# Kernel optimization log

Hardware: AMD Instinct MI355X
Metric: run time of the kernel (lower is better)

## Reference

```python
import jax, jax.numpy as jnp
import numpy as np

N_AGENTS = 8; N_DUMMY = 16; BATCH = 1024; PLAN = 128; HID = 256

def setup_inputs():
    key = jax.random.key(0)
    ks = jax.random.split(key, 12)
    N, ND, B, P, H = N_AGENTS, N_DUMMY, BATCH, PLAN, HID
    plans = jax.random.normal(ks[0], (B, N, P), jnp.float32)
    keep = jax.random.bernoulli(ks[1], 0.7, (B, N))  # ragged communication pattern
    comm_plans = jax.random.normal(ks[2], (B, N, P), jnp.float32) * keep[:, :, None]
    coord_hiddens = 0.1 * jax.random.normal(ks[3], (N, 2, B, H), jnp.float32)
    dummy_noise = jax.random.normal(ks[4], (N, ND - N, B, 2 * P), jnp.float32)
    s = 0.05
    Wi_f = s * jax.random.normal(ks[5], (N, 3 * H, 2 * P), jnp.float32)
    Wh_f = s * jax.random.normal(ks[6], (N, 3 * H, H), jnp.float32)
    Wi_b = s * jax.random.normal(ks[7], (N, 3 * H, 2 * P), jnp.float32)
    Wh_b = s * jax.random.normal(ks[8], (N, 3 * H, H), jnp.float32)
    ln_g = jnp.ones((N, 2 * H), jnp.float32)
    ln_b = jnp.zeros((N, 2 * H), jnp.float32)
    W1 = s * jax.random.normal(ks[9], (N, H, 2 * H), jnp.float32)
    b1 = jnp.zeros((N, H), jnp.float32)
    W2 = s * jax.random.normal(ks[10], (N, 2, H), jnp.float32)
    b2 = jnp.zeros((N, 2), jnp.float32)
    return dict(plans=plans, comm_plans=comm_plans, coord_hiddens=coord_hiddens,
                dummy_noise=dummy_noise, Wi_f=Wi_f, Wh_f=Wh_f, Wi_b=Wi_b, Wh_b=Wh_b,
                ln_g=ln_g, ln_b=ln_b, W1=W1, b1=b1, W2=W2, b2=b2)

def _gru_scan(xs, h0, Wi, Wh, valid):
    # PyTorch GRU cell (biases are zero-initialized in RecurrentHead), length-masked
    H = h0.shape[-1]
    gi_all = jnp.einsum('tbi,gi->tbg', xs, Wi)  # (T,B,3H) input projections, one GEMM
    def step(h, inp):
        gi, v = inp
        gh = h @ Wh.T
        r = jax.nn.sigmoid(gi[:, :H] + gh[:, :H])
        z = jax.nn.sigmoid(gi[:, H:2 * H] + gh[:, H:2 * H])
        n = jnp.tanh(gi[:, 2 * H:] + r * gh[:, 2 * H:])
        hn = (1.0 - z) * n + z * h
        h = jnp.where(v[:, None], hn, h)            # packed: no update past seq end
        return h, jnp.where(v[:, None], hn, 0.0)    # pad_packed returns zeros there
    hT, out = jax.lax.scan(step, h0, (gi_all, valid))
    return out, hT

def _forward(plans, comm_plans, coord_hiddens, dummy_noise, Wi_f, Wh_f, Wi_b, Wh_b, ln_g, ln_b, W1, b1, W2, b2):
    B, N, P = plans.shape
    ND = N_DUMMY
    # comm_plans[~any(any(comm_plans))] = plans[...]
    empty = ~jnp.any(jnp.any(comm_plans != 0, -1), -1)            # (B,)
    comm = jnp.where(empty[:, None, None], plans, comm_plans)     # (B,N,P)
    mask_real = jnp.any(comm != 0, -1).T                          # (N,B)
    mask = jnp.concatenate([mask_real, jnp.ones((ND - N, B), bool)], 0)  # (ND,B)
    mask_flat = mask.reshape(-1)
    seq_len = mask.sum(0)                                         # (B,)
    t_idx = jnp.arange(ND)[:, None]
    packed_mask = t_idx < seq_len[None, :]                        # (ND,B)
    pm_flat = packed_mask.reshape(-1)
    # torch boolean-index / masked_scatter consume elements in flat row-major order;
    # we reproduce those exact semantics.
    src_idx = jnp.nonzero(mask_flat, size=ND * B, fill_value=0)[0]
    rank_pack = jnp.cumsum(pm_flat) - 1
    cum_scat = jnp.cumsum(mask_flat) - 1
    rev_idx = jnp.where(packed_mask, seq_len[None, :] - 1 - t_idx, 0)

    def pack(x):  # compact_seq[packed_mask] = x[batch_mask]
        xf = x.reshape(ND * B, -1)
        return jnp.where(pm_flat[:, None], xf[src_idx[rank_pack]], 0.0).reshape(ND, B, -1)

    def scatter(s):  # zeros.masked_scatter(mask, scores)
        st, sb = cum_scat // B, cum_scat % B
        return jnp.where(mask_flat[:, None], s[st, sb], 0.0).reshape(ND, B, -1)

    def rev(a):  # per-column reversal within valid length (for bidirectional GRU)
        g = jnp.take_along_axis(a, jnp.broadcast_to(rev_idx[:, :, None], a.shape), axis=0)
        return jnp.where(packed_mask[:, :, None], g, 0.0)

    plans_t = plans.transpose(1, 0, 2)  # (N,B,P): plans[:, i] per agent

    def per_agent(plan_i, dn_i, hxs_i, wif, whf, wib, whb, g, bta, w1, bb1, w2, bb2):
        others = jnp.concatenate([jnp.broadcast_to(plan_i[:, None, :], comm.shape), comm], -1)  # (B,N,2P)
        x = jnp.concatenate([others.transpose(1, 0, 2), dn_i], 0)  # (ND,B,2P) with randn dummy rows
        cseq = pack(x)
        out_f, hf = _gru_scan(cseq, hxs_i[0], wif, whf, packed_mask)
        out_b_r, hb = _gru_scan(rev(cseq), hxs_i[1], wib, whb, packed_mask)
        out_b = rev(out_b_r)
        scores = scatter(jnp.concatenate([out_f, out_b], -1))  # (ND,B,2H)
        mu = scores.mean(-1, keepdims=True)
        var = ((scores - mu) ** 2).mean(-1, keepdims=True)
        scores = (scores - mu) * jax.lax.rsqrt(var + 1e-5) * g + bta  # LayerNorm
        h1 = jax.nn.relu(jnp.einsum('tbc,hc->tbh', scores, w1) + bb1)
        cm = jnp.einsum('tbh,oh->tbo', h1, w2) + bb2               # (ND,B,2)
        return cm, jnp.stack([hf, hb])                              # (2,B,H)

    coord_masks, coord_rnn_hxs = jax.vmap(per_agent)(
        plans_t, dummy_noise, coord_hiddens, Wi_f, Wh_f, Wi_b, Wh_b, ln_g, ln_b, W1, b1, W2, b2)
    return coord_masks, coord_rnn_hxs

def reference(plans, comm_plans, coord_hiddens, dummy_noise, Wi_f, Wh_f, Wi_b, Wh_b, ln_g, ln_b, W1, b1, W2, b2):
    return _forward(plans, comm_plans, coord_hiddens, dummy_noise, Wi_f, Wh_f, Wi_b, Wh_b, ln_g, ln_b, W1, b1, W2, b2)
```

## Files before the change

### kernel.cpp

```cpp
#include <hip/hip_runtime.h>


typedef _Float16 f16;
typedef __attribute__((ext_vector_type(4))) _Float16 f16x4;
typedef __attribute__((ext_vector_type(8))) _Float16 f16x8;
typedef __attribute__((ext_vector_type(4))) float floatx4;

__device__ __forceinline__ float sigf(float x) { return 1.0f / (1.0f + __expf(-x)); }
__device__ __forceinline__ float tanhfast(float x) {
    float e = __expf(2.0f * x);
    return 1.0f - 2.0f / (e + 1.0f);
}

__device__ __forceinline__ void gl16(const f16* g, f16* l) {
    __builtin_amdgcn_global_load_lds((const __attribute__((address_space(1))) void*)g,
                                     (__attribute__((address_space(3))) void*)l,
                                     16, 0, 0);
}

__global__ void k_empty(const float* __restrict__ comm, int* __restrict__ empty) {
    int b = blockIdx.x;
    __shared__ int flag;
    if (threadIdx.x == 0) flag = 0;
    __syncthreads();
    const float* p = comm + (size_t)b * 1024;
    int any = 0;
    for (int e = threadIdx.x; e < 1024; e += 256)
        if (p[e] != 0.0f) any = 1;
    if (any) flag = 1;
    __syncthreads();
    if (threadIdx.x == 0) empty[b] = (flag == 0);
}

__global__ void k_mask(const float* __restrict__ plans, const float* __restrict__ comm,
                       const int* __restrict__ empty, int* __restrict__ mask) {
    int row = blockIdx.x * 4 + (threadIdx.x >> 6);
    int lane = threadIdx.x & 63;
    int t = row >> 10, b = row & 1023;
    int m;
    if (t >= 8) {
        m = 1;
    } else {
        const float* src = (empty[b] ? plans : comm) + ((size_t)b * 8 + t) * 128;
        float v0 = src[lane * 2], v1 = src[lane * 2 + 1];
        m = __any((v0 != 0.0f) || (v1 != 0.0f)) ? 1 : 0;
    }
    if (lane == 0) mask[row] = m;
}

__global__ void k_scan(const int* __restrict__ mask, int* __restrict__ seq_len,
                       int* __restrict__ pack_src, int* __restrict__ scat_src,
                       int* __restrict__ inv_scat) {
    __shared__ int s_sl[1024];
    __shared__ int s_m[1024];
    __shared__ int s_p[1024];
    __shared__ unsigned short s_idx[16384];
    int tid = threadIdx.x;
    int sl = 8;
    for (int t = 0; t < 8; t++) sl += mask[t * 1024 + tid];
    s_sl[tid] = sl;
    seq_len[tid] = sl;
    __syncthreads();
    int mv[16], pv[16];
    int mc = 0, pc = 0;
    int j0 = tid * 16;
    for (int q = 0; q < 16; q++) {
        int j = j0 + q;
        mv[q] = mask[j];
        pv[q] = ((j >> 10) < s_sl[j & 1023]) ? 1 : 0;
        mc += mv[q]; pc += pv[q];
    }
    s_m[tid] = mc; s_p[tid] = pc;
    __syncthreads();
    for (int off = 1; off < 1024; off <<= 1) {
        int am = (tid >= off) ? s_m[tid - off] : 0;
        int ap = (tid >= off) ? s_p[tid - off] : 0;
        __syncthreads();
        s_m[tid] += am; s_p[tid] += ap;
        __syncthreads();
    }
    if (tid == 1023) seq_len[1024] = s_m[1023];
    int moff = s_m[tid] - mc;
    int poff = s_p[tid] - pc;
    int rm = moff;
    for (int q = 0; q < 16; q++)
        if (mv[q]) s_idx[rm++] = (unsigned short)(j0 + q);
    __syncthreads();
    rm = moff;
    int rp = poff;
    for (int q = 0; q < 16; q++) {
        int j = j0 + q;
        scat_src[j] = mv[q] ? rm : -1;
        if (mv[q]) { inv_scat[rm] = j; rm++; }
        pack_src[j] = pv[q] ? (int)s_idx[rp] : -1;
        if (pv[q]) rp++;
    }
}

__global__ void k_pack(const float* __restrict__ plans, const float* __restrict__ comm,
                       const float* __restrict__ dummy, const int* __restrict__ empty,
                       const int* __restrict__ pack_src, f16* __restrict__ cseq) {
    int row = blockIdx.x * 8 + (threadIdx.x >> 5);
    int lane = threadIdx.x & 31;
    int i = row >> 14;
    int j = row & 16383;
    int s = pack_src[j];
    f16x8 o = {0, 0, 0, 0, 0, 0, 0, 0};
    if (s >= 0) {
        int tp = s >> 10, bp = s & 1023;
        const float* src;
        if (tp < 8) {
            if (lane < 16) src = plans + ((size_t)bp * 8 + i) * 128 + lane * 8;
            else src = (empty[bp] ? plans : comm) + ((size_t)bp * 8 + tp) * 128 + (lane - 16) * 8;
        } else {
            src = dummy + (((size_t)i * 8 + (tp - 8)) * 1024 + bp) * 256 + lane * 8;
        }
        float4 v0 = *(const float4*)src;
        float4 v1 = *(const float4*)(src + 4);
        o[0] = (f16)v0.x; o[1] = (f16)v0.y; o[2] = (f16)v0.z; o[3] = (f16)v0.w;
        o[4] = (f16)v1.x; o[5] = (f16)v1.y; o[6] = (f16)v1.z; o[7] = (f16)v1.w;
    }
    *(f16x8*)(cseq + ((size_t)row << 8) + lane * 8) = o;
}

__global__ void k_prep_w(const float* __restrict__ Wi_f, const float* __restrict__ Wh_f,
                         const float* __restrict__ Wi_b, const float* __restrict__ Wh_b,
                         f16* __restrict__ whalf) {
    int ch2 = blockIdx.y;
    int ch = ch2 >> 1, sel = ch2 & 1;
    int i = ch >> 1, d = ch & 1;
    const float* src = sel ? (d ? Wh_b : Wh_f) : (d ? Wi_b : Wi_f);
    src += (size_t)i * 196608;
    int off = (blockIdx.x * 256 + threadIdx.x) * 4;
    float4 v = *(const float4*)(src + off);
    f16x4 o = { (f16)v.x, (f16)v.y, (f16)v.z, (f16)v.w };
    *(f16x4*)(whalf + (size_t)ch2 * 196608 + off) = o;
}

__global__ void k_prep_w1(const float* __restrict__ W1, f16* __restrict__ w1half) {
    int off = (blockIdx.x * 256 + threadIdx.x) * 4;
    float4 v = *(const float4*)(W1 + off);
    f16x4 o = { (f16)v.x, (f16)v.y, (f16)v.z, (f16)v.w };
    *(f16x4*)(w1half + off) = o;
}

__global__ void k_init_h(const float* __restrict__ hx, float* __restrict__ h,
                         f16* __restrict__ hh0) {
    int e = (blockIdx.x * 256 + threadIdx.x) * 4;
    float4 v = *(const float4*)(hx + e);
    *(float4*)(h + e) = v;
    f16x4 o = { (f16)v.x, (f16)v.y, (f16)v.z, (f16)v.w };
    *(f16x4*)(hh0 + e) = o;
}

__global__ void k_zfill(const int* __restrict__ scat_src, const int* __restrict__ seq_len,
                        f16* __restrict__ scores) {
    int j = blockIdx.x;
    int tid = threadIdx.x;
    int c = scat_src[j];
    if (c < 0) {
        for (int i = 0; i < 8; i++) {
            unsigned int* p = (unsigned int*)(scores + ((size_t)(i * 16384 + j)) * 512);
            p[tid] = 0u;
        }
    } else {
        int st = c >> 10, sb = c & 1023;
        if (st >= seq_len[sb] && tid < 128) {
            for (int i = 0; i < 8; i++) {
                unsigned int* p = (unsigned int*)(scores + ((size_t)(i * 16384 + j)) * 512 + 256);
                p[tid] = 0u;
            }
        }
    }
}

__global__ __launch_bounds__(256, 2) void k_step(
    const f16* __restrict__ cseq, const f16* __restrict__ whalf,
    float* __restrict__ h, const f16* __restrict__ hh_in, f16* __restrict__ hh_out,
    f16* __restrict__ scores, const int* __restrict__ seq_len,
    const int* __restrict__ inv_scat, int t)
{
    __shared__ f16 lA[128 * 64];
    __shared__ f16 lB[192 * 64];
    int bx = blockIdx.x;
    int ch = bx >> 5;
    int mt = (bx >> 2) & 7;
    int nt = bx & 3;
    int i = ch >> 1, d = ch & 1;
    int tid = threadIdx.x;
    int lane = tid & 63, w = tid >> 6;
    int li = lane & 15, q = lane >> 4;
    int rsub = lane >> 3;
    int sc = (lane & 7) ^ rsub;

    const f16* pA[4]; const f16* pH[4]; const f16* pB[6];
#pragma unroll
    for (int p = 0; p < 4; p++) {
        int ar = (w * 4 + p) * 8 + rsub;
        int b = mt * 128 + ar;
        int tt = t;
        if (d) { int sl = seq_len[b]; tt = sl - 1 - t; if (tt < 0) tt = 0; }
        pA[p] = cseq + (((size_t)i * 16 + tt) * 1024 + b) * 256 + sc * 8;
        pH[p] = hh_in + ((size_t)ch * 1024 + b) * 256 + sc * 8;
    }
#pragma unroll
    for (int p = 0; p < 6; p++) {
        int nr = (w * 6 + p) * 8 + rsub;
        int g = (nr >> 6) * 256 + nt * 64 + (nr & 63);
        pB[p] = whalf + (size_t)(ch * 2) * 196608 + (size_t)g * 256 + sc * 8;
    }

    floatx4 accr[4][2], accz[4][2], accgi[4][2], accgh[4][2];
    floatx4 z4 = {0.f, 0.f, 0.f, 0.f};
#pragma unroll
    for (int n = 0; n < 4; n++)
        for (int s = 0; s < 2; s++) { accr[n][s] = z4; accz[n][s] = z4; accgi[n][s] = z4; accgh[n][s] = z4; }

    for (int kt = 0; kt < 512; kt += 64) {
        bool xph = (kt < 256);
        if (xph) {
#pragma unroll
            for (int p = 0; p < 4; p++) gl16(pA[p] + kt, &lA[(w * 4 + p) * 512]);
#pragma unroll
            for (int p = 0; p < 6; p++) gl16(pB[p] + kt, &lB[(w * 6 + p) * 512]);
        } else {
#pragma unroll
            for (int p = 0; p < 4; p++) gl16(pH[p] + (kt - 256), &lA[(w * 4 + p) * 512]);
#pragma unroll
            for (int p = 0; p < 6; p++) gl16(pB[p] + 196608 + (kt - 256), &lB[(w * 6 + p) * 512]);
        }
        __syncthreads();
#pragma unroll
        for (int kk = 0; kk < 64; kk += 32) {
            int sw = ((q + (kk >> 3)) ^ (li & 7)) << 3;
            f16x8 a0 = *(f16x8*)&lA[(w * 32 + li) * 64 + sw];
            f16x8 a1 = *(f16x8*)&lA[(w * 32 + 16 + li) * 64 + sw];
#pragma unroll
            for (int n = 0; n < 4; n++) {
                f16x8 br = *(f16x8*)&lB[(n * 16 + li) * 64 + sw];
                f16x8 bz = *(f16x8*)&lB[(64 + n * 16 + li) * 64 + sw];
                f16x8 bn = *(f16x8*)&lB[(128 + n * 16 + li) * 64 + sw];
                accr[n][0] = __builtin_amdgcn_mfma_f32_16x16x32_f16(a0, br, accr[n][0], 0, 0, 0);
                accr[n][1] = __builtin_amdgcn_mfma_f32_16x16x32_f16(a1, br, accr[n][1], 0, 0, 0);
                accz[n][0] = __builtin_amdgcn_mfma_f32_16x16x32_f16(a0, bz, accz[n][0], 0, 0, 0);
                accz[n][1] = __builtin_amdgcn_mfma_f32_16x16x32_f16(a1, bz, accz[n][1], 0, 0, 0);
                if (xph) {
                    accgi[n][0] = __builtin_amdgcn_mfma_f32_16x16x32_f16(a0, bn, accgi[n][0], 0, 0, 0);
                    accgi[n][1] = __builtin_amdgcn_mfma_f32_16x16x32_f16(a1, bn, accgi[n][1], 0, 0, 0);
                } else {
                    accgh[n][0] = __builtin_amdgcn_mfma_f32_16x16x32_f16(a0, bn, accgh[n][0], 0, 0, 0);
                    accgh[n][1] = __builtin_amdgcn_mfma_f32_16x16x32_f16(a1, bn, accgh[n][1], 0, 0, 0);
                }
            }
        }
        __syncthreads();
    }

    int T = seq_len[1024];
#pragma unroll
    for (int s = 0; s < 2; s++) {
#pragma unroll
        for (int r = 0; r < 4; r++) {
            int b = mt * 128 + w * 32 + s * 16 + q * 4 + r;
            int sl = seq_len[b];
            int v = (t < sl);
            int st = d ? (sl - 1 - t) : t;
            int cfl = st * 1024 + b;
            int j = -1;
            if (d == 0) { if (cfl < T) j = inv_scat[cfl]; }
            else        { if (v && cfl < T) j = inv_scat[cfl]; }
#pragma unroll
            for (int n = 0; n < 4; n++) {
                int c = nt * 64 + n * 16 + li;
                float rg = sigf(accr[n][s][r]);
                float zg = sigf(accz[n][s][r]);
                float nn = tanhfast(accgi[n][s][r] + rg * accgh[n][s][r]);
                size_t hidx = ((size_t)ch * 1024 + b) * 256 + c;
                float hp = h[hidx];
                float hn = (1.0f - zg) * nn + zg * hp;
                float hnew = v ? hn : hp;
                h[hidx] = hnew;
                hh_out[hidx] = (f16)hnew;
                if (j >= 0)
                    scores[((size_t)(i * 16384 + j)) * 512 + d * 256 + c] = (f16)(v ? hn : 0.0f);
            }
        }
    }
}

__global__ __launch_bounds__(512, 4) void k_mlp(
    const f16* __restrict__ scores,
    const float* __restrict__ ln_g, const float* __restrict__ ln_b,
    const f16* __restrict__ w1half, const float* __restrict__ b1,
    const float* __restrict__ W2, const float* __restrict__ b2,
    float* __restrict__ out)
{
    __shared__ f16 lA[128 * 64];
    __shared__ f16 lB[256 * 64];
    __shared__ float s_mu[128], s_rs[128];
    int bx = blockIdx.x;
    int i = bx >> 7, mt = bx & 127;
    int tid = threadIdx.x, lane = tid & 63, w = tid >> 6, li = lane & 15, q = lane >> 4;
    int rsub = lane >> 3;
    int sc = (lane & 7) ^ rsub;

    {
        int r = tid >> 2, sub = tid & 3;
        const f16* sp = scores + ((size_t)(i * 16384 + mt * 128 + r)) * 512 + sub * 128;
        float s = 0.f, sq = 0.f;
#pragma unroll
        for (int e = 0; e < 16; e++) {
            uint4 raw = *(const uint4*)(sp + e * 8);
            f16x8 v = *(f16x8*)&raw;
#pragma unroll
            for (int u = 0; u < 8; u++) { float f = (float)v[u]; s += f; sq += f * f; }
        }
        s += __shfl_xor(s, 1); sq += __shfl_xor(sq, 1);
        s += __shfl_xor(s, 2); sq += __shfl_xor(sq, 2);
        if (sub == 0) {
            float mu = s * (1.0f / 512.0f);
            float var = sq * (1.0f / 512.0f) - mu * mu;
            if (var < 0.f) var = 0.f;
            s_mu[r] = mu;
            s_rs[r] = rsqrtf(var + 1e-5f);
        }
    }

    const f16* pB[4];
#pragma unroll
    for (int p = 0; p < 4; p++) {
        int nr = (w * 4 + p) * 8 + rsub;
        pB[p] = w1half + ((size_t)i * 256 + nr) * 512 + sc * 8;
    }

    floatx4 acc[16];
    floatx4 z4 = {0.f, 0.f, 0.f, 0.f};
#pragma unroll
    for (int n = 0; n < 16; n++) acc[n] = z4;
    __syncthreads();

    for (int kt = 0; kt < 512; kt += 64) {
#pragma unroll
        for (int p = 0; p < 2; p++) {
            int e = p * 512 + tid;
            int ar = e >> 3, chk = e & 7;
            int m = mt * 128 + ar;
            uint4 raw = *(const uint4*)(scores + ((size_t)(i * 16384 + m)) * 512 + kt + chk * 8);
            f16x8 sv = *(f16x8*)&raw;
            float mu = s_mu[ar], rs = s_rs[ar];
            int co = i * 512 + kt + chk * 8;
            float4 g0 = *(const float4*)(ln_g + co);
            float4 g1 = *(const float4*)(ln_g + co + 4);
            float4 t0 = *(const float4*)(ln_b + co);
            float4 t1 = *(const float4*)(ln_b + co + 4);
            f16x8 ov;
            ov[0] = (f16)(((float)sv[0] - mu) * rs * g0.x + t0.x);
            ov[1] = (f16)(((float)sv[1] - mu) * rs * g0.y + t0.y);
            ov[2] = (f16)(((float)sv[2] - mu) * rs * g0.z + t0.z);
            ov[3] = (f16)(((float)sv[3] - mu) * rs * g0.w + t0.w);
            ov[4] = (f16)(((float)sv[4] - mu) * rs * g1.x + t1.x);
            ov[5] = (f16)(((float)sv[5] - mu) * rs * g1.y + t1.y);
            ov[6] = (f16)(((float)sv[6] - mu) * rs * g1.z + t1.z);
            ov[7] = (f16)(((float)sv[7] - mu) * rs * g1.w + t1.w);
            *(f16x8*)&lA[ar * 64 + ((chk ^ (ar & 7)) << 3)] = ov;
        }
#pragma unroll
        for (int p = 0; p < 4; p++) gl16(pB[p] + kt, &lB[(w * 4 + p) * 512]);
        __syncthreads();
#pragma unroll
        for (int kk = 0; kk < 64; kk += 32) {
            int sw = ((q + (kk >> 3)) ^ (li & 7)) << 3;
            f16x8 a = *(f16x8*)&lA[(w * 16 + li) * 64 + sw];
#pragma unroll
            for (int n = 0; n < 16; n++) {
                f16x8 bb = *(f16x8*)&lB[(n * 16 + li) * 64 + sw];
                acc[n] = __builtin_amdgcn_mfma_f32_16x16x32_f16(a, bb, acc[n], 0, 0, 0);
            }
        }
        __syncthreads();
    }

    float b1v[16], w2a[16], w2b[16];
#pragma unroll
    for (int n = 0; n < 16; n++) {
        int col = n * 16 + li;
        b1v[n] = b1[i * 256 + col];
        w2a[n] = W2[((size_t)i * 2 + 0) * 256 + col];
        w2b[n] = W2[((size_t)i * 2 + 1) * 256 + col];
    }
    float b2a = b2[i * 2], b2b = b2[i * 2 + 1];
#pragma unroll
    for (int r = 0; r < 4; r++) {
        float p0 = 0.f, p1 = 0.f;
#pragma unroll
        for (int n = 0; n < 16; n++) {
            float h1 = acc[n][r] + b1v[n];
            h1 = fmaxf(h1, 0.0f);
            p0 += h1 * w2a[n];
            p1 += h1 * w2b[n];
        }
#pragma unroll
        for (int off = 1; off < 16; off <<= 1) { p0 += __shfl_xor(p0, off); p1 += __shfl_xor(p1, off); }
        if (li == 0) {
            int m = mt * 128 + w * 16 + q * 4 + r;
            size_t oi = ((size_t)i * 16384 + m) * 2;
            out[oi]     = p0 + b2a;
            out[oi + 1] = p1 + b2b;
        }
    }
}

__global__ void k_hout(const float* __restrict__ h, float* __restrict__ out) {
    int e = (blockIdx.x * 256 + threadIdx.x) * 4;
    *(float4*)(out + 262144 + e) = *(const float4*)(h + e);
}

extern "C" void kernel_launch(void* const* d_in, const int* in_sizes, int n_in,
                              void* d_out, int out_size, void* d_ws, size_t ws_size,
                              hipStream_t stream)
{
    const float* plans = (const float*)d_in[0];
    const float* comm  = (const float*)d_in[1];
    const float* hx    = (const float*)d_in[2];
    const float* dummy = (const float*)d_in[3];
    const float* Wi_f  = (const float*)d_in[4];
    const float* Wh_f  = (const float*)d_in[5];
    const float* Wi_b  = (const float*)d_in[6];
    const float* Wh_b  = (const float*)d_in[7];
    const float* ln_g  = (const float*)d_in[8];
    const float* ln_b  = (const float*)d_in[9];
    const float* W1    = (const float*)d_in[10];
    const float* b1    = (const float*)d_in[11];
    const float* W2    = (const float*)d_in[12];
    const float* b2    = (const float*)d_in[13];
    float* out = (float*)d_out;

    char* ws = (char*)d_ws;
    f16*    cseq    = (f16*)   (ws + 0);
    f16*    scores  = (f16*)   (ws + 67108864);
    float*  h       = (float*) (ws + 201326592);
    f16*    hh0     = (f16*)   (ws + 218103808);
    f16*    hh1     = (f16*)   (ws + 226492416);
    f16*    whalf   = (f16*)   (ws + 234881024);
    f16*    w1half  = (f16*)   (ws + 247463936);
    int*    empty   = (int*)   (ws + 250609664);
    int*    seq_len = (int*)   (ws + 250613760);
    int*    maskb   = (int*)   (ws + 250621952);
    int*    pack_s  = (int*)   (ws + 250687488);
    int*    scat_s  = (int*)   (ws + 250753024);
    int*    inv_s   = (int*)   (ws + 250818560);
    if (ws_size < 250884096ULL) return;

    k_empty<<<1024, 256, 0, stream>>>(comm, empty);
    k_mask<<<4096, 256, 0, stream>>>(plans, comm, empty, maskb);
    k_scan<<<1, 1024, 0, stream>>>(maskb, seq_len, pack_s, scat_s, inv_s);
    k_pack<<<16384, 256, 0, stream>>>(plans, comm, dummy, empty, pack_s, cseq);
    k_zfill<<<16384, 256, 0, stream>>>(scat_s, seq_len, scores);
    k_prep_w<<<dim3(192, 32), 256, 0, stream>>>(Wi_f, Wh_f, Wi_b, Wh_b, whalf);
    k_prep_w1<<<1024, 256, 0, stream>>>(W1, w1half);
    k_init_h<<<4096, 256, 0, stream>>>(hx, h, hh0);
    for (int t = 0; t < 16; t++) {
        f16* hin  = (t & 1) ? hh1 : hh0;
        f16* hout = (t & 1) ? hh0 : hh1;
        k_step<<<512, 256, 0, stream>>>(cseq, whalf, h, hin, hout, scores,
                                        seq_len, inv_s, t);
    }
    k_mlp<<<1024, 512, 0, stream>>>(scores, ln_g, ln_b, w1half, b1, W2, b2, out);
    k_hout<<<4096, 256, 0, stream>>>(h, out);
}
```

Before: 793.2 us.

## Fuse GRU timesteps into one persistent kernel and fold LayerNorm into W1

New measurement: 1.336 ms. +68.4%, slower.

```diff
diff --git a/kernel.cpp b/kernel.cpp
--- a/kernel.cpp
+++ b/kernel.cpp
@@ -137,20 +137,35 @@
     *(f16x4*)(whalf + (size_t)ch2 * 196608 + off) = o;
 }
 
-__global__ void k_prep_w1(const float* __restrict__ W1, f16* __restrict__ w1half) {
+__global__ void k_prep_w1(const float* __restrict__ W1, const float* __restrict__ ln_g,
+                          f16* __restrict__ w1g) {
     int off = (blockIdx.x * 256 + threadIdx.x) * 4;
+    int i = off >> 17;
+    int c = off & 511;
     float4 v = *(const float4*)(W1 + off);
-    f16x4 o = { (f16)v.x, (f16)v.y, (f16)v.z, (f16)v.w };
-    *(f16x4*)(w1half + off) = o;
-}
-
-__global__ void k_init_h(const float* __restrict__ hx, float* __restrict__ h,
-                         f16* __restrict__ hh0) {
-    int e = (blockIdx.x * 256 + threadIdx.x) * 4;
-    float4 v = *(const float4*)(hx + e);
-    *(float4*)(h + e) = v;
-    f16x4 o = { (f16)v.x, (f16)v.y, (f16)v.z, (f16)v.w };
-    *(f16x4*)(hh0 + e) = o;
+    float4 g = *(const float4*)(ln_g + i * 512 + c);
+    f16x4 o = { (f16)(v.x * g.x), (f16)(v.y * g.y), (f16)(v.z * g.z), (f16)(v.w * g.w) };
+    *(f16x4*)(w1g + off) = o;
+}
+
+__global__ void k_prep_c(const float* __restrict__ W1, const float* __restrict__ ln_g,
+                         const float* __restrict__ ln_b, const float* __restrict__ b1,
+                         float* __restrict__ wsum, float* __restrict__ c1) {
+    int row = blockIdx.x * 4 + (threadIdx.x >> 6);
+    int lane = threadIdx.x & 63;
+    int i = row >> 8;
+    const float* src = W1 + (size_t)row * 512;
+    float s1 = 0.f, s2 = 0.f;
+#pragma unroll
+    for (int e = 0; e < 8; e++) {
+        int c = lane * 8 + e;
+        float wv = src[c];
+        s1 += (float)(f16)(wv * ln_g[i * 512 + c]);
+        s2 += wv * ln_b[i * 512 + c];
+    }
+#pragma unroll
+    for (int off = 1; off < 64; off <<= 1) { s1 += __shfl_xor(s1, off); s2 += __shfl_xor(s2, off); }
+    if (lane == 0) { wsum[row] = s1; c1[row] = s2 + b1[row]; }
 }
 
 __global__ void k_zfill(const int* __restrict__ scat_src, const int* __restrict__ seq_len,
@@ -174,124 +189,176 @@
     }
 }
 
-__global__ __launch_bounds__(256, 2) void k_step(
+__global__ __launch_bounds__(512, 2) void k_gru(
     const f16* __restrict__ cseq, const f16* __restrict__ whalf,
-    float* __restrict__ h, const f16* __restrict__ hh_in, f16* __restrict__ hh_out,
-    f16* __restrict__ scores, const int* __restrict__ seq_len,
-    const int* __restrict__ inv_scat, int t)
+    const float* __restrict__ hx, f16* __restrict__ scores,
+    const int* __restrict__ seq_len, const int* __restrict__ inv_scat,
+    float* __restrict__ out)
 {
-    __shared__ f16 lA[128 * 64];
+    __shared__ f16 lH[64 * 256];
     __shared__ f16 lB[192 * 64];
     int bx = blockIdx.x;
-    int ch = bx >> 5;
-    int mt = (bx >> 2) & 7;
-    int nt = bx & 3;
+    int ch = bx & 15, mseg = bx >> 4;
     int i = ch >> 1, d = ch & 1;
     int tid = threadIdx.x;
     int lane = tid & 63, w = tid >> 6;
     int li = lane & 15, q = lane >> 4;
-    int rsub = lane >> 3;
-    int sc = (lane & 7) ^ rsub;
-
-    const f16* pA[4]; const f16* pH[4]; const f16* pB[6];
-#pragma unroll
-    for (int p = 0; p < 4; p++) {
-        int ar = (w * 4 + p) * 8 + rsub;
-        int b = mt * 128 + ar;
-        int tt = t;
-        if (d) { int sl = seq_len[b]; tt = sl - 1 - t; if (tt < 0) tt = 0; }
-        pA[p] = cseq + (((size_t)i * 16 + tt) * 1024 + b) * 256 + sc * 8;
-        pH[p] = hh_in + ((size_t)ch * 1024 + b) * 256 + sc * 8;
-    }
-#pragma unroll
-    for (int p = 0; p < 6; p++) {
-        int nr = (w * 6 + p) * 8 + rsub;
-        int g = (nr >> 6) * 256 + nt * 64 + (nr & 63);
-        pB[p] = whalf + (size_t)(ch * 2) * 196608 + (size_t)g * 256 + sc * 8;
-    }
-
-    floatx4 accr[4][2], accz[4][2], accgi[4][2], accgh[4][2];
-    floatx4 z4 = {0.f, 0.f, 0.f, 0.f};
-#pragma unroll
-    for (int n = 0; n < 4; n++)
-        for (int s = 0; s < 2; s++) { accr[n][s] = z4; accz[n][s] = z4; accgi[n][s] = z4; accgh[n][s] = z4; }
-
-    for (int kt = 0; kt < 512; kt += 64) {
-        bool xph = (kt < 256);
-        if (xph) {
-#pragma unroll
-            for (int p = 0; p < 4; p++) gl16(pA[p] + kt, &lA[(w * 4 + p) * 512]);
-#pragma unroll
-            for (int p = 0; p < 6; p++) gl16(pB[p] + kt, &lB[(w * 6 + p) * 512]);
-        } else {
-#pragma unroll
-            for (int p = 0; p < 4; p++) gl16(pH[p] + (kt - 256), &lA[(w * 4 + p) * 512]);
-#pragma unroll
-            for (int p = 0; p < 6; p++) gl16(pB[p] + 196608 + (kt - 256), &lB[(w * 6 + p) * 512]);
-        }
-        __syncthreads();
-#pragma unroll
-        for (int kk = 0; kk < 64; kk += 32) {
-            int sw = ((q + (kk >> 3)) ^ (li & 7)) << 3;
-            f16x8 a0 = *(f16x8*)&lA[(w * 32 + li) * 64 + sw];
-            f16x8 a1 = *(f16x8*)&lA[(w * 32 + 16 + li) * 64 + sw];
-#pragma unroll
-            for (int n = 0; n < 4; n++) {
-                f16x8 br = *(f16x8*)&lB[(n * 16 + li) * 64 + sw];
-                f16x8 bz = *(f16x8*)&lB[(64 + n * 16 + li) * 64 + sw];
-                f16x8 bn = *(f16x8*)&lB[(128 + n * 16 + li) * 64 + sw];
-                accr[n][0] = __builtin_amdgcn_mfma_f32_16x16x32_f16(a0, br, accr[n][0], 0, 0, 0);
-                accr[n][1] = __builtin_amdgcn_mfma_f32_16x16x32_f16(a1, br, accr[n][1], 0, 0, 0);
-                accz[n][0] = __builtin_amdgcn_mfma_f32_16x16x32_f16(a0, bz, accz[n][0], 0, 0, 0);
-                accz[n][1] = __builtin_amdgcn_mfma_f32_16x16x32_f16(a1, bz, accz[n][1], 0, 0, 0);
-                if (xph) {
-                    accgi[n][0] = __builtin_amdgcn_mfma_f32_16x16x32_f16(a0, bn, accgi[n][0], 0, 0, 0);
-                    accgi[n][1] = __builtin_amdgcn_mfma_f32_16x16x32_f16(a1, bn, accgi[n][1], 0, 0, 0);
-                } else {
-                    accgh[n][0] = __builtin_amdgcn_mfma_f32_16x16x32_f16(a0, bn, accgh[n][0], 0, 0, 0);
-                    accgh[n][1] = __builtin_amdgcn_mfma_f32_16x16x32_f16(a1, bn, accgh[n][1], 0, 0, 0);
+    int rg = w >> 2, ct = w & 3;
+
+    int sl_frag[2], sl_epi[2][4];
+#pragma unroll
+    for (int s = 0; s < 2; s++) {
+        sl_frag[s] = seq_len[mseg * 64 + rg * 32 + s * 16 + li];
+#pragma unroll
+        for (int r = 0; r < 4; r++)
+            sl_epi[s][r] = seq_len[mseg * 64 + rg * 32 + s * 16 + q * 4 + r];
+    }
+    int T = seq_len[1024];
+
+    float h_reg[4][2][4];
+#pragma unroll
+    for (int nt = 0; nt < 4; nt++)
+#pragma unroll
+        for (int s = 0; s < 2; s++)
+#pragma unroll
+            for (int r = 0; r < 4; r++) {
+                int row = rg * 32 + s * 16 + q * 4 + r;
+                int c = nt * 64 + ct * 16 + li;
+                float v = hx[((size_t)ch * 1024 + mseg * 64 + row) * 256 + c];
+                h_reg[nt][s][r] = v;
+                int chunk = c >> 3;
+                int chs = (chunk & 24) | ((chunk ^ row) & 7);
+                lH[row * 256 + chs * 8 + (c & 7)] = (f16)v;
+            }
+
+    const f16* wbase = whalf + (size_t)ch * 393216;
+    int nrp[3], ckp[3];
+#pragma unroll
+    for (int p = 0; p < 3; p++) {
+        int e = p * 512 + tid;
+        nrp[p] = e >> 3;
+        ckp[p] = (e & 7) ^ (nrp[p] & 7);
+    }
+    __syncthreads();
+
+#pragma unroll 1
+    for (int t = 0; t < 16; t++) {
+        f16x8 xf[4][2][2];
+#pragma unroll
+        for (int s = 0; s < 2; s++) {
+            int b = mseg * 64 + rg * 32 + s * 16 + li;
+            int tt = t;
+            if (d) { tt = sl_frag[s] - 1 - t; if (tt < 0) tt = 0; }
+            const f16* xrow = cseq + (((size_t)i * 16 + tt) * 1024 + b) * 256;
+#pragma unroll
+            for (int kt4 = 0; kt4 < 4; kt4++)
+#pragma unroll
+                for (int kk = 0; kk < 2; kk++)
+                    xf[kt4][kk][s] = *(const f16x8*)(xrow + kt4 * 64 + kk * 32 + q * 8);
+        }
+
+#pragma unroll
+        for (int nt = 0; nt < 4; nt++) {
+            floatx4 ar_[2], az_[2], agi_[2], agh_[2];
+            floatx4 z4 = {0.f, 0.f, 0.f, 0.f};
+            ar_[0] = z4; ar_[1] = z4; az_[0] = z4; az_[1] = z4;
+            agi_[0] = z4; agi_[1] = z4; agh_[0] = z4; agh_[1] = z4;
+#pragma unroll
+            for (int kt8 = 0; kt8 < 8; kt8++) {
+                const int xph = (kt8 < 4);
+                const int kofs = xph ? kt8 * 64 : (kt8 - 4) * 64;
+                const f16* wsrc = wbase + (xph ? 0 : 196608);
+#pragma unroll
+                for (int p = 0; p < 3; p++) {
+                    int nr = nrp[p];
+                    int g = (nr >> 6) * 256 + nt * 64 + (nr & 63);
+                    gl16(wsrc + (size_t)g * 256 + kofs + ckp[p] * 8, &lB[p * 4096 + w * 512]);
+                }
+                __syncthreads();
+#pragma unroll
+                for (int kk = 0; kk < 2; kk++) {
+                    int bofs = ((kk * 4 + q) ^ (li & 7)) << 3;
+                    f16x8 br = *(f16x8*)&lB[(ct * 16 + li) * 64 + bofs];
+                    f16x8 bz = *(f16x8*)&lB[(64 + ct * 16 + li) * 64 + bofs];
+                    f16x8 bn = *(f16x8*)&lB[(128 + ct * 16 + li) * 64 + bofs];
+                    f16x8 a0, a1;
+                    if (xph) {
+                        a0 = xf[kt8][kk][0];
+                        a1 = xf[kt8][kk][1];
+                    } else {
+                        int hofs = (((kt8 - 4) * 8) | ((kk * 4 + q) ^ (li & 7))) << 3;
+                        a0 = *(f16x8*)&lH[(rg * 32 + li) * 256 + hofs];
+                        a1 = *(f16x8*)&lH[(rg * 32 + 16 + li) * 256 + hofs];
+                    }
+                    ar_[0] = __builtin_amdgcn_mfma_f32_16x16x32_f16(a0, br, ar_[0], 0, 0, 0);
+                    ar_[1] = __builtin_amdgcn_mfma_f32_16x16x32_f16(a1, br, ar_[1], 0, 0, 0);
+                    az_[0] = __builtin_amdgcn_mfma_f32_16x16x32_f16(a0, bz, az_[0], 0, 0, 0);
+                    az_[1] = __builtin_amdgcn_mfma_f32_16x16x32_f16(a1, bz, az_[1], 0, 0, 0);
+                    if (xph) {
+                        agi_[0] = __builtin_amdgcn_mfma_f32_16x16x32_f16(a0, bn, agi_[0], 0, 0, 0);
+                        agi_[1] = __builtin_amdgcn_mfma_f32_16x16x32_f16(a1, bn, agi_[1], 0, 0, 0);
+                    } else {
+                        agh_[0] = __builtin_amdgcn_mfma_f32_16x16x32_f16(a0, bn, agh_[0], 0, 0, 0);
+                        agh_[1] = __builtin_amdgcn_mfma_f32_16x16x32_f16(a1, bn, agh_[1], 0, 0, 0);
+                    }
+                }
+                __syncthreads();
+            }
+#pragma unroll
+            for (int s = 0; s < 2; s++) {
+#pragma unroll
+                for (int r = 0; r < 4; r++) {
+                    int b = mseg * 64 + rg * 32 + s * 16 + q * 4 + r;
+                    int sl = sl_epi[s][r];
+                    int v = (t < sl);
+                    int st = d ? (sl - 1 - t) : t;
+                    int cfl = st * 1024 + b;
+                    int j = -1;
+                    if (d == 0) { if (cfl < T) j = inv_scat[cfl]; }
+                    else        { if (v && cfl < T) j = inv_scat[cfl]; }
+                    float rgt = sigf(ar_[s][r]);
+                    float zgt = sigf(az_[s][r]);
+                    float nn = tanhfast(agi_[s][r] + rgt * agh_[s][r]);
+                    float hp = h_reg[nt][s][r];
+                    float hn = (1.0f - zgt) * nn + zgt * hp;
+                    h_reg[nt][s][r] = v ? hn : hp;
+                    if (j >= 0) {
+                        int c = nt * 64 + ct * 16 + li;
+                        scores[((size_t)(i * 16384 + j)) * 512 + d * 256 + c] = (f16)(v ? hn : 0.0f);
+                    }
                 }
             }
         }
+#pragma unroll
+        for (int nt = 0; nt < 4; nt++)
+#pragma unroll
+            for (int s = 0; s < 2; s++)
+#pragma unroll
+                for (int r = 0; r < 4; r++) {
+                    int row = rg * 32 + s * 16 + q * 4 + r;
+                    int c = nt * 64 + ct * 16 + li;
+                    int chunk = c >> 3;
+                    int chs = (chunk & 24) | ((chunk ^ row) & 7);
+                    lH[row * 256 + chs * 8 + (c & 7)] = (f16)h_reg[nt][s][r];
+                }
         __syncthreads();
     }
 
-    int T = seq_len[1024];
-#pragma unroll
-    for (int s = 0; s < 2; s++) {
-#pragma unroll
-        for (int r = 0; r < 4; r++) {
-            int b = mt * 128 + w * 32 + s * 16 + q * 4 + r;
-            int sl = seq_len[b];
-            int v = (t < sl);
-            int st = d ? (sl - 1 - t) : t;
-            int cfl = st * 1024 + b;
-            int j = -1;
-            if (d == 0) { if (cfl < T) j = inv_scat[cfl]; }
-            else        { if (v && cfl < T) j = inv_scat[cfl]; }
-#pragma unroll
-            for (int n = 0; n < 4; n++) {
-                int c = nt * 64 + n * 16 + li;
-                float rg = sigf(accr[n][s][r]);
-                float zg = sigf(accz[n][s][r]);
-                float nn = tanhfast(accgi[n][s][r] + rg * accgh[n][s][r]);
-                size_t hidx = ((size_t)ch * 1024 + b) * 256 + c;
-                float hp = h[hidx];
-                float hn = (1.0f - zg) * nn + zg * hp;
-                float hnew = v ? hn : hp;
-                h[hidx] = hnew;
-                hh_out[hidx] = (f16)hnew;
-                if (j >= 0)
-                    scores[((size_t)(i * 16384 + j)) * 512 + d * 256 + c] = (f16)(v ? hn : 0.0f);
+#pragma unroll
+    for (int nt = 0; nt < 4; nt++)
+#pragma unroll
+        for (int s = 0; s < 2; s++)
+#pragma unroll
+            for (int r = 0; r < 4; r++) {
+                int b = mseg * 64 + rg * 32 + s * 16 + q * 4 + r;
+                int c = nt * 64 + ct * 16 + li;
+                out[262144 + ((size_t)ch * 1024 + b) * 256 + c] = h_reg[nt][s][r];
             }
-        }
-    }
 }
 
 __global__ __launch_bounds__(512, 4) void k_mlp(
-    const f16* __restrict__ scores,
-    const float* __restrict__ ln_g, const float* __restrict__ ln_b,
-    const f16* __restrict__ w1half, const float* __restrict__ b1,
+    const f16* __restrict__ scores, const f16* __restrict__ w1g,
+    const float* __restrict__ wsum, const float* __restrict__ c1v,
     const float* __restrict__ W2, const float* __restrict__ b2,
     float* __restrict__ out)
 {
@@ -326,11 +393,17 @@
         }
     }
 
-    const f16* pB[4];
+    const f16* pA[2]; const f16* pB[4];
+#pragma unroll
+    for (int p = 0; p < 2; p++) {
+        int e = p * 512 + tid;
+        int ar = e >> 3, chunk = e & 7;
+        pA[p] = scores + ((size_t)(i * 16384 + mt * 128 + ar)) * 512 + ((chunk ^ (ar & 7)) * 8);
+    }
 #pragma unroll
     for (int p = 0; p < 4; p++) {
         int nr = (w * 4 + p) * 8 + rsub;
-        pB[p] = w1half + ((size_t)i * 256 + nr) * 512 + sc * 8;
+        pB[p] = w1g + ((size_t)i * 256 + nr) * 512 + sc * 8;
     }
 
     floatx4 acc[16];
@@ -341,29 +414,7 @@
 
     for (int kt = 0; kt < 512; kt += 64) {
 #pragma unroll
-        for (int p = 0; p < 2; p++) {
-            int e = p * 512 + tid;
-            int ar = e >> 3, chk = e & 7;
-            int m = mt * 128 + ar;
-            uint4 raw = *(const uint4*)(scores + ((size_t)(i * 16384 + m)) * 512 + kt + chk * 8);
-            f16x8 sv = *(f16x8*)&raw;
-            float mu = s_mu[ar], rs = s_rs[ar];
-            int co = i * 512 + kt + chk * 8;
-            float4 g0 = *(const float4*)(ln_g + co);
-            float4 g1 = *(const float4*)(ln_g + co + 4);
-            float4 t0 = *(const float4*)(ln_b + co);
-            float4 t1 = *(const float4*)(ln_b + co + 4);
-            f16x8 ov;
-            ov[0] = (f16)(((float)sv[0] - mu) * rs * g0.x + t0.x);
-            ov[1] = (f16)(((float)sv[1] - mu) * rs * g0.y + t0.y);
-            ov[2] = (f16)(((float)sv[2] - mu) * rs * g0.z + t0.z);
-            ov[3] = (f16)(((float)sv[3] - mu) * rs * g0.w + t0.w);
-            ov[4] = (f16)(((float)sv[4] - mu) * rs * g1.x + t1.x);
-            ov[5] = (f16)(((float)sv[5] - mu) * rs * g1.y + t1.y);
-            ov[6] = (f16)(((float)sv[6] - mu) * rs * g1.z + t1.z);
-            ov[7] = (f16)(((float)sv[7] - mu) * rs * g1.w + t1.w);
-            *(f16x8*)&lA[ar * 64 + ((chk ^ (ar & 7)) << 3)] = ov;
-        }
+        for (int p = 0; p < 2; p++) gl16(pA[p] + kt, &lA[p * 4096 + w * 512]);
 #pragma unroll
         for (int p = 0; p < 4; p++) gl16(pB[p] + kt, &lB[(w * 4 + p) * 512]);
         __syncthreads();
@@ -380,21 +431,24 @@
         __syncthreads();
     }
 
-    float b1v[16], w2a[16], w2b[16];
+    float wsv[16], c1r[16], w2a[16], w2b[16];
 #pragma unroll
     for (int n = 0; n < 16; n++) {
         int col = n * 16 + li;
-        b1v[n] = b1[i * 256 + col];
+        wsv[n] = wsum[i * 256 + col];
+        c1r[n] = c1v[i * 256 + col];
         w2a[n] = W2[((size_t)i * 2 + 0) * 256 + col];
         w2b[n] = W2[((size_t)i * 2 + 1) * 256 + col];
     }
     float b2a = b2[i * 2], b2b = b2[i * 2 + 1];
 #pragma unroll
     for (int r = 0; r < 4; r++) {
+        int ml = w * 16 + q * 4 + r;
+        float mu = s_mu[ml], rs = s_rs[ml];
         float p0 = 0.f, p1 = 0.f;
 #pragma unroll
         for (int n = 0; n < 16; n++) {
-            float h1 = acc[n][r] + b1v[n];
+            float h1 = rs * (acc[n][r] - mu * wsv[n]) + c1r[n];
             h1 = fmaxf(h1, 0.0f);
             p0 += h1 * w2a[n];
             p1 += h1 * w2b[n];
@@ -402,17 +456,12 @@
 #pragma unroll
         for (int off = 1; off < 16; off <<= 1) { p0 += __shfl_xor(p0, off); p1 += __shfl_xor(p1, off); }
         if (li == 0) {
-            int m = mt * 128 + w * 16 + q * 4 + r;
+            int m = mt * 128 + ml;
             size_t oi = ((size_t)i * 16384 + m) * 2;
             out[oi]     = p0 + b2a;
             out[oi + 1] = p1 + b2b;
         }
     }
-}
-
-__global__ void k_hout(const float* __restrict__ h, float* __restrict__ out) {
-    int e = (blockIdx.x * 256 + threadIdx.x) * 4;
-    *(float4*)(out + 262144 + e) = *(const float4*)(h + e);
 }
 
 extern "C" void kernel_launch(void* const* d_in, const int* in_sizes, int n_in,
@@ -438,18 +487,17 @@
     char* ws = (char*)d_ws;
     f16*    cseq    = (f16*)   (ws + 0);
     f16*    scores  = (f16*)   (ws + 67108864);
-    float*  h       = (float*) (ws + 201326592);
-    f16*    hh0     = (f16*)   (ws + 218103808);
-    f16*    hh1     = (f16*)   (ws + 226492416);
-    f16*    whalf   = (f16*)   (ws + 234881024);
-    f16*    w1half  = (f16*)   (ws + 247463936);
-    int*    empty   = (int*)   (ws + 250609664);
-    int*    seq_len = (int*)   (ws + 250613760);
-    int*    maskb   = (int*)   (ws + 250621952);
-    int*    pack_s  = (int*)   (ws + 250687488);
-    int*    scat_s  = (int*)   (ws + 250753024);
-    int*    inv_s   = (int*)   (ws + 250818560);
-    if (ws_size < 250884096ULL) return;
+    f16*    whalf   = (f16*)   (ws + 201326592);
+    f16*    w1g     = (f16*)   (ws + 213909504);
+    float*  wsum    = (float*) (ws + 216006656);
+    float*  c1v     = (float*) (ws + 216014848);
+    int*    empty   = (int*)   (ws + 216023040);
+    int*    seq_len = (int*)   (ws + 216027136);
+    int*    maskb   = (int*)   (ws + 216035328);
+    int*    pack_s  = (int*)   (ws + 216100864);
+    int*    scat_s  = (int*)   (ws + 216166400);
+    int*    inv_s   = (int*)   (ws + 216231936);
+    if (ws_size < 216297472ULL) return;
 
     k_empty<<<1024, 256, 0, stream>>>(comm, empty);
     k_mask<<<4096, 256, 0, stream>>>(plans, comm, empty, maskb);
@@ -457,14 +505,8 @@
     k_pack<<<16384, 256, 0, stream>>>(plans, comm, dummy, empty, pack_s, cseq);
     k_zfill<<<16384, 256, 0, stream>>>(scat_s, seq_len, scores);
     k_prep_w<<<dim3(192, 32), 256, 0, stream>>>(Wi_f, Wh_f, Wi_b, Wh_b, whalf);
-    k_prep_w1<<<1024, 256, 0, stream>>>(W1, w1half);
-    k_init_h<<<4096, 256, 0, stream>>>(hx, h, hh0);
-    for (int t = 0; t < 16; t++) {
-        f16* hin  = (t & 1) ? hh1 : hh0;
-        f16* hout = (t & 1) ? hh0 : hh1;
-        k_step<<<512, 256, 0, stream>>>(cseq, whalf, h, hin, hout, scores,
-                                        seq_len, inv_s, t);
-    }
-    k_mlp<<<1024, 512, 0, stream>>>(scores, ln_g, ln_b, w1half, b1, W2, b2, out);
-    k_hout<<<4096, 256, 0, stream>>>(h, out);
-}
+    k_prep_w1<<<1024, 256, 0, stream>>>(W1, ln_g, w1g);
+    k_prep_c<<<512, 256, 0, stream>>>(W1, ln_g, ln_b, b1, wsum, c1v);
+    k_gru<<<256, 512, 0, stream>>>(cseq, whalf, hx, scores, seq_len, inv_s, out);
+    k_mlp<<<1024, 512, 0, stream>>>(scores, w1g, wsum, c1v, W2, b2, out);
+}
```
